# Kernel optimization log

Measured on AMD Instinct MI355X. Metric: run time of the kernel, lower is better.

## Reference

```python
import jax, jax.numpy as jnp
import numpy as np
from jax import lax
from jax.scipy.special import logsumexp

EPS = 0.01 ** 2      # blur^p, geomloss SamplesLoss(p=2, blur=0.01)
N_ITERS = 20         # fixed Sinkhorn iterations (log-domain)


def setup_inputs() -> dict:
    key = jax.random.key(0)
    k1, k2 = jax.random.split(key)
    p_q = jax.random.normal(k1, (4, 4096, 3), dtype=jnp.float32)
    p_gt = jax.random.normal(k2, (4, 4096, 4), dtype=jnp.float32)
    return {"p_q": p_q, "p_gt": p_gt}


def _cost(x, y):
    # C_ij = 0.5 * ||x_i - y_j||^2   (geomloss p=2 convention), [B,N,M]
    x2 = jnp.sum(x * x, -1)
    y2 = jnp.sum(y * y, -1)
    xy = jnp.einsum('bnd,bmd->bnm', x, y)
    return 0.5 * (x2[:, :, None] + y2[:, None, :] - 2.0 * xy)


def _softmin(C, pot, logw, axis):
    # -eps * logsumexp over `axis` of (pot - C)/eps + logw ; pot/logw broadcast on `axis`'s dual
    if axis == 2:
        z = (pot[:, None, :] - C) / EPS + logw  # reduce over M -> [B,N]
    else:
        z = (pot[:, :, None] - C) / EPS + logw  # reduce over N -> [B,M]
    return -EPS * logsumexp(z, axis=axis)


def _ot_potentials(C, loga, logb):
    # asymmetric log-domain Sinkhorn; iterate on detached cost (envelope theorem,
    # matching geomloss' detach-then-extrapolate gradient), final differentiable step.
    Cd = lax.stop_gradient(C)
    B, N, M = C.shape

    def body(i, fg):
        f, g = fg
        f = _softmin(Cd, g, logb, axis=2)
        g = _softmin(Cd, f, loga, axis=1)
        return (f, g)

    f0 = jnp.zeros((B, N), C.dtype)
    g0 = jnp.zeros((B, M), C.dtype)
    f, g = lax.fori_loop(0, N_ITERS, body, (f0, g0))
    fd, gd = lax.stop_gradient(f), lax.stop_gradient(g)
    f = _softmin(C, gd, logb, axis=2)
    g = _softmin(C, fd, loga, axis=1)
    return f, g


def _sym_potential(C, logw):
    # symmetric Sinkhorn for OT(a,a): single potential, damped updates
    Cd = lax.stop_gradient(C)
    B, N, _ = C.shape

    def body(i, f):
        return 0.5 * (f + _softmin(Cd, f, logw, axis=2))

    f = lax.fori_loop(0, N_ITERS, body, jnp.zeros((B, N), C.dtype))
    return _softmin(C, lax.stop_gradient(f), logw, axis=2)


def reference(p_q, p_gt):
    x = p_q                 # [B,N,3]
    y = p_gt[:, :, :3]      # [B,M,3]
    B, N, _ = x.shape
    M = y.shape[1]
    loga = jnp.full((1, 1), -jnp.log(N), x.dtype)  # uniform weights (broadcast)
    logb = jnp.full((1, 1), -jnp.log(M), x.dtype)

    Cxy = _cost(x, y)
    Cxx = _cost(x, x)
    Cyy = _cost(y, y)

    f_ab, g_ab = _ot_potentials(Cxy, loga[:, :, None] * 0 - jnp.log(N), logb)
    # note: loga used in softmin over N-axis needs [.., :, None] broadcast; build explicitly:
    loga_b = jnp.full((B, N, 1), -jnp.log(N), x.dtype)
    logb_b = jnp.full((B, 1, M), -jnp.log(M), x.dtype)
    f_ab = _softmin(Cxy, lax.stop_gradient(g_ab), logb_b, axis=2)  # idempotent re-extrapolation
    g_ab = _softmin(Cxy, lax.stop_gradient(f_ab), loga_b, axis=1)
    f_aa = _sym_potential(Cxx, jnp.full((B, 1, N), -jnp.log(N), x.dtype))
    g_bb = _sym_potential(Cyy, logb_b)

    # debiased Sinkhorn divergence per batch: <a, f_ab - f_aa> + <b, g_ab - g_bb>
    L = jnp.mean(f_ab - f_aa, axis=1) + jnp.mean(g_ab - g_bb, axis=1)
    return L
```

## Files before the change

### kernel.cpp

```cpp
#include <hip/hip_runtime.h>
#include <math.h>

#define NPTS 4096
#define NBATCH 4
#define BLOCK 512
#define RPW 8

static constexpr float KSCALE     = 1.4426950408889634f / 1e-4f;
static constexpr float INVK2      = 1.0f / (KSCALE * KSCALE);
static constexpr float EPSLN2     = 1e-4f * 0.6931471805599453f;
static constexpr float NEGEPSLOGW = 8.31776616671934e-4f;
static constexpr float THR        = 20.0f;

__device__ __forceinline__ float fexp2(float x){
#if __has_builtin(__builtin_amdgcn_exp2f)
  return __builtin_amdgcn_exp2f(x);
#else
  return exp2f(x);
#endif
}
__device__ __forceinline__ float flog2(float x){
#if __has_builtin(__builtin_amdgcn_logf)
  return __builtin_amdgcn_logf(x);
#else
  return log2f(x);
#endif
}
__device__ __forceinline__ float frl(float x){
  return __int_as_float(__builtin_amdgcn_readfirstlane(__float_as_int(x)));
}

__global__ __launch_bounds__(BLOCK, 4) void softmin_kernel(
    const float* __restrict__ rowA, int rsA, const float4* __restrict__ pkInA,
    float4* __restrict__ pkOutA, const float* __restrict__ hOldA,
    float* __restrict__ outA, int modeA,
    const float* __restrict__ rowB, int rsB, const float4* __restrict__ pkInB,
    float4* __restrict__ pkOutB, const float* __restrict__ hOldB,
    float* __restrict__ outB, int modeB)
{
  __shared__ float4 qs[NPTS];

  int bid = blockIdx.x;
  const float* rowp; const float4* pkin; float4* pkout; const float* hold;
  float* outp; int rs, mode;
  if (bid < 256) { rowp=rowA; pkin=pkInA; pkout=pkOutA; hold=hOldA; outp=outA; rs=rsA; mode=modeA; }
  else           { rowp=rowB; pkin=pkInB; pkout=pkOutB; hold=hOldB; outp=outB; rs=rsB; mode=modeB; }
  int lb = bid & 255;
  int b  = lb >> 6;
  int rb = lb & 63;

  int tid = threadIdx.x;
  int lane = tid & 63;
  int wu = __builtin_amdgcn_readfirstlane(tid >> 6);
  int r0 = rb*64 + wu*RPW;
  int ridx0 = b*NPTS + r0;

  {
    const float4* src = pkin + b*NPTS;
    #pragma unroll
    for (int i = 0; i < NPTS/BLOCK; ++i)
      qs[i*BLOCK + tid] = src[i*BLOCK + tid];
  }

  float sx[RPW], sy[RPW], sz[RPW];
  #pragma unroll
  for (int i = 0; i < RPW; ++i) {
    const float* p = rowp + (size_t)(ridx0 + i) * rs;
    sx[i] = frl(p[0]*KSCALE); sy[i] = frl(p[1]*KSCALE); sz[i] = frl(p[2]*KSCALE);
  }

  __syncthreads();

  float cmax[4][RPW];
  #pragma unroll
  for (int c = 0; c < 4; ++c)
    #pragma unroll
    for (int r = 0; r < RPW; ++r) cmax[c][r] = -INFINITY;

  #pragma unroll
  for (int c = 0; c < 4; ++c) {
    #pragma unroll
    for (int g = 0; g < 4; ++g) {
      int base = c*1024 + g*256 + lane;
      float4 q0 = qs[base], q1 = qs[base+64], q2 = qs[base+128], q3 = qs[base+192];
      #pragma unroll
      for (int r = 0; r < RPW; ++r) {
        float t0 = fmaf(sx[r],q0.x,fmaf(sy[r],q0.y,fmaf(sz[r],q0.z,q0.w)));
        float t1 = fmaf(sx[r],q1.x,fmaf(sy[r],q1.y,fmaf(sz[r],q1.z,q1.w)));
        float t2 = fmaf(sx[r],q2.x,fmaf(sy[r],q2.y,fmaf(sz[r],q2.z,q2.w)));
        float t3 = fmaf(sx[r],q3.x,fmaf(sy[r],q3.y,fmaf(sz[r],q3.z,q3.w)));
        float u  = fmaxf(fmaxf(t0,t1),t2);
        cmax[c][r] = fmaxf(fmaxf(u,t3),cmax[c][r]);
      }
    }
  }

  float M[RPW];
  #pragma unroll
  for (int r = 0; r < RPW; ++r) {
    float mm = fmaxf(fmaxf(cmax[0][r],cmax[1][r]), fmaxf(cmax[2][r],cmax[3][r]));
    #pragma unroll
    for (int off = 32; off; off >>= 1) mm = fmaxf(mm, __shfl_xor(mm, off, 64));
    M[r] = mm;
  }

  float S[RPW];
  #pragma unroll
  for (int r = 0; r < RPW; ++r) S[r] = 0.f;

  #pragma unroll
  for (int c = 0; c < 4; ++c) {
    int am = 0;
    #pragma unroll
    for (int r = 0; r < RPW; ++r)
      am |= __any(cmax[c][r] > M[r] - THR) ? (1 << r) : 0;
    if (am) {
      #pragma unroll
      for (int g = 0; g < 4; ++g) {
        int base = c*1024 + g*256 + lane;
        float4 q0 = qs[base], q1 = qs[base+64], q2 = qs[base+128], q3 = qs[base+192];
        #pragma unroll
        for (int r = 0; r < RPW; ++r) if (am & (1 << r)) {
          float t0 = fmaf(sx[r],q0.x,fmaf(sy[r],q0.y,fmaf(sz[r],q0.z,q0.w)));
          float t1 = fmaf(sx[r],q1.x,fmaf(sy[r],q1.y,fmaf(sz[r],q1.z,q1.w)));
          float t2 = fmaf(sx[r],q2.x,fmaf(sy[r],q2.y,fmaf(sz[r],q2.z,q2.w)));
          float t3 = fmaf(sx[r],q3.x,fmaf(sy[r],q3.y,fmaf(sz[r],q3.z,q3.w)));
          float u  = fmaxf(fmaxf(t0,t1),t2);
          float v  = fmaxf(u,t3);
          if (__any(v > M[r] - THR)) {
            float e0 = fexp2(t0-M[r]) + fexp2(t1-M[r]);
            float e1 = fexp2(t2-M[r]) + fexp2(t3-M[r]);
            S[r] += e0 + e1;
          }
        }
      }
    }
  }

  #pragma unroll
  for (int r = 0; r < RPW; ++r) {
    float s = S[r];
    #pragma unroll
    for (int off = 32; off; off >>= 1) s += __shfl_xor(s, off, 64);
    float ch = 0.5f*(sx[r]*sx[r] + sy[r]*sy[r] + sz[r]*sz[r]) * INVK2;
    float res = fmaf(-EPSLN2, M[r] + flog2(s), ch + NEGEPSLOGW);
    if (lane == r) {
      if (mode) res = 0.5f*(hold[ridx0 + r] + res);
      outp[ridx0 + r] = res;
      ((float*)(pkout + (ridx0 + r)))[3] = (res - ch) * KSCALE;
    }
  }
}

__global__ void pack_init(const float* __restrict__ x, const float* __restrict__ y,
                          float4* pkfab, float4* pkgab,
                          float4* pkfaa0, float4* pkfaa1,
                          float4* pkgbb0, float4* pkgbb1)
{
  int i = blockIdx.x*256 + threadIdx.x;
  const float* xp = x + (size_t)i*3;
  float xx = xp[0], xy = xp[1], xz = xp[2];
  float4 vx; vx.x=xx; vx.y=xy; vx.z=xz;
  vx.w = -0.5f*(xx*xx + xy*xy + xz*xz)*KSCALE;
  const float* yp = y + (size_t)i*4;
  float yx = yp[0], yy = yp[1], yz = yp[2];
  float4 vy; vy.x=yx; vy.y=yy; vy.z=yz;
  vy.w = -0.5f*(yx*yx + yy*yy + yz*yz)*KSCALE;
  pkgab[i]  = vx; pkfaa0[i] = vx; pkfaa1[i] = vx;
  pkfab[i]  = vy; pkgbb0[i] = vy; pkgbb1[i] = vy;
}

__global__ void reduce_kernel(const float* __restrict__ fab, const float* __restrict__ faa,
                              const float* __restrict__ gab, const float* __restrict__ gbb,
                              float* __restrict__ out)
{
  int b = blockIdx.x;
  int tid = threadIdx.x;
  float s = 0.f;
  for (int i = tid; i < NPTS; i += 256) {
    int idx = b*NPTS + i;
    s += (fab[idx] - faa[idx]) + (gab[idx] - gbb[idx]);
  }
  for (int off = 32; off > 0; off >>= 1) s += __shfl_down(s, off, 64);
  __shared__ float red[4];
  if ((tid & 63) == 0) red[tid >> 6] = s;
  __syncthreads();
  if (tid == 0) out[b] = (red[0]+red[1]+red[2]+red[3]) * (1.0f/NPTS);
}

extern "C" void kernel_launch(void* const* d_in, const int* in_sizes, int n_in,
                              void* d_out, int out_size, void* d_ws, size_t ws_size,
                              hipStream_t stream)
{
  const float* x = (const float*)d_in[0];
  const float* y = (const float*)d_in[1];
  float* ws = (float*)d_ws;
  const size_t P = (size_t)NBATCH * NPTS;

  float* f_ab    = ws + 0*P;
  float* g_ab    = ws + 1*P;
  float* faaR[2] = { ws + 2*P, ws + 4*P };
  float* gbbR[2] = { ws + 3*P, ws + 5*P };
  float4* pk4    = (float4*)(ws + 6*P);
  float4* PKfab    = pk4 + 0*P;
  float4* PKgab    = pk4 + 1*P;
  float4* PKfaa[2] = { pk4 + 2*P, pk4 + 3*P };
  float4* PKgbb[2] = { pk4 + 4*P, pk4 + 5*P };

  hipMemsetAsync(ws + 2*P, 0, 2*P*sizeof(float), stream);
  pack_init<<<dim3(P/256), dim3(256), 0, stream>>>(x, y, PKfab, PKgab,
                                                   PKfaa[0], PKfaa[1], PKgbb[0], PKgbb[1]);

  for (int i = 0; i < 21; ++i) {
    int cur = i & 1, nxt = cur ^ 1;
    int modeS = (i < 20) ? 1 : 0;
    softmin_kernel<<<512, BLOCK, 0, stream>>>(
        x, 3, PKfab, PKgab, f_ab, f_ab, 0,
        x, 3, PKfaa[cur], PKfaa[nxt], faaR[cur], faaR[nxt], modeS);
    softmin_kernel<<<512, BLOCK, 0, stream>>>(
        y, 4, PKgab, PKfab, g_ab, g_ab, 0,
        y, 4, PKgbb[cur], PKgbb[nxt], gbbR[cur], gbbR[nxt], modeS);
  }
  reduce_kernel<<<dim3(4), dim3(256), 0, stream>>>(f_ab, faaR[1], g_ab, gbbR[1], (float*)d_out);
}
```

Before: 1.013 ms.

## Use single-pass online softmin seeded by previous potential for symmetric blocks

Blocks handling the symmetric self-transport potentials (bid >= 256) now run a single pass. The running max is seeded from the previous potential plus the point's norm term, and an online rescaled logsumexp skips tiles whose values fall below the threshold. This replaces the separate max pass followed by an exp pass, cutting the dot-product work roughly in half for those blocks. The risk is that a loose initial max estimate adds rescale exps, and the lane-divergent online max needs a cross-lane rescale at the end.

After: 910.7 us, median of 2. 1.11x faster.

```diff
diff --git a/kernel.cpp b/kernel.cpp
--- a/kernel.cpp
+++ b/kernel.cpp
@@ -62,26 +62,108 @@
       qs[i*BLOCK + tid] = src[i*BLOCK + tid];
   }
 
-  float sx[RPW], sy[RPW], sz[RPW];
+  float sx[RPW], sy[RPW], sz[RPW], hh[RPW];
   #pragma unroll
   for (int i = 0; i < RPW; ++i) {
     const float* p = rowp + (size_t)(ridx0 + i) * rs;
     sx[i] = frl(p[0]*KSCALE); sy[i] = frl(p[1]*KSCALE); sz[i] = frl(p[2]*KSCALE);
+    hh[i] = frl(hold[ridx0 + i]);
   }
 
   __syncthreads();
 
-  float cmax[4][RPW];
-  #pragma unroll
-  for (int c = 0; c < 4; ++c)
-    #pragma unroll
-    for (int r = 0; r < RPW; ++r) cmax[c][r] = -INFINITY;
-
-  #pragma unroll
-  for (int c = 0; c < 4; ++c) {
-    #pragma unroll
-    for (int g = 0; g < 4; ++g) {
-      int base = c*1024 + g*256 + lane;
+  if (bid < 256) {
+    float cmax[4][RPW];
+    #pragma unroll
+    for (int c = 0; c < 4; ++c)
+      #pragma unroll
+      for (int r = 0; r < RPW; ++r) cmax[c][r] = -INFINITY;
+
+    #pragma unroll
+    for (int c = 0; c < 4; ++c) {
+      #pragma unroll
+      for (int g = 0; g < 4; ++g) {
+        int base = c*1024 + g*256 + lane;
+        float4 q0 = qs[base], q1 = qs[base+64], q2 = qs[base+128], q3 = qs[base+192];
+        #pragma unroll
+        for (int r = 0; r < RPW; ++r) {
+          float t0 = fmaf(sx[r],q0.x,fmaf(sy[r],q0.y,fmaf(sz[r],q0.z,q0.w)));
+          float t1 = fmaf(sx[r],q1.x,fmaf(sy[r],q1.y,fmaf(sz[r],q1.z,q1.w)));
+          float t2 = fmaf(sx[r],q2.x,fmaf(sy[r],q2.y,fmaf(sz[r],q2.z,q2.w)));
+          float t3 = fmaf(sx[r],q3.x,fmaf(sy[r],q3.y,fmaf(sz[r],q3.z,q3.w)));
+          float u  = fmaxf(fmaxf(t0,t1),t2);
+          cmax[c][r] = fmaxf(fmaxf(u,t3),cmax[c][r]);
+        }
+      }
+    }
+
+    float M[RPW];
+    #pragma unroll
+    for (int r = 0; r < RPW; ++r) {
+      float mm = fmaxf(fmaxf(cmax[0][r],cmax[1][r]), fmaxf(cmax[2][r],cmax[3][r]));
+      #pragma unroll
+      for (int off = 32; off; off >>= 1) mm = fmaxf(mm, __shfl_xor(mm, off, 64));
+      M[r] = mm;
+    }
+
+    float S[RPW];
+    #pragma unroll
+    for (int r = 0; r < RPW; ++r) S[r] = 0.f;
+
+    #pragma unroll
+    for (int c = 0; c < 4; ++c) {
+      int am = 0;
+      #pragma unroll
+      for (int r = 0; r < RPW; ++r)
+        am |= __any(cmax[c][r] > M[r] - THR) ? (1 << r) : 0;
+      if (am) {
+        #pragma unroll
+        for (int g = 0; g < 4; ++g) {
+          int base = c*1024 + g*256 + lane;
+          float4 q0 = qs[base], q1 = qs[base+64], q2 = qs[base+128], q3 = qs[base+192];
+          #pragma unroll
+          for (int r = 0; r < RPW; ++r) if (am & (1 << r)) {
+            float t0 = fmaf(sx[r],q0.x,fmaf(sy[r],q0.y,fmaf(sz[r],q0.z,q0.w)));
+            float t1 = fmaf(sx[r],q1.x,fmaf(sy[r],q1.y,fmaf(sz[r],q1.z,q1.w)));
+            float t2 = fmaf(sx[r],q2.x,fmaf(sy[r],q2.y,fmaf(sz[r],q2.z,q2.w)));
+            float t3 = fmaf(sx[r],q3.x,fmaf(sy[r],q3.y,fmaf(sz[r],q3.z,q3.w)));
+            float u  = fmaxf(fmaxf(t0,t1),t2);
+            float v  = fmaxf(u,t3);
+            if (__any(v > M[r] - THR)) {
+              float e0 = fexp2(t0-M[r]) + fexp2(t1-M[r]);
+              float e1 = fexp2(t2-M[r]) + fexp2(t3-M[r]);
+              S[r] += e0 + e1;
+            }
+          }
+        }
+      }
+    }
+
+    #pragma unroll
+    for (int r = 0; r < RPW; ++r) {
+      float s = S[r];
+      #pragma unroll
+      for (int off = 32; off; off >>= 1) s += __shfl_xor(s, off, 64);
+      float ch = 0.5f*(sx[r]*sx[r] + sy[r]*sy[r] + sz[r]*sz[r]) * INVK2;
+      float res = fmaf(-EPSLN2, M[r] + flog2(s), ch + NEGEPSLOGW);
+      if (lane == r) {
+        if (mode) res = 0.5f*(hh[r] + res);
+        outp[ridx0 + r] = res;
+        ((float*)(pkout + (ridx0 + r)))[3] = (res - ch) * KSCALE;
+      }
+    }
+  } else {
+    float M[RPW], S[RPW], chv[RPW];
+    #pragma unroll
+    for (int r = 0; r < RPW; ++r) {
+      chv[r] = 0.5f*(sx[r]*sx[r] + sy[r]*sy[r] + sz[r]*sz[r]) * INVK2;
+      M[r] = (hh[r] + chv[r]) * KSCALE;
+      S[r] = 0.f;
+    }
+
+    #pragma unroll
+    for (int g = 0; g < 16; ++g) {
+      int base = g*256 + lane;
       float4 q0 = qs[base], q1 = qs[base+64], q2 = qs[base+128], q3 = qs[base+192];
       #pragma unroll
       for (int r = 0; r < RPW; ++r) {
@@ -89,65 +171,33 @@
         float t1 = fmaf(sx[r],q1.x,fmaf(sy[r],q1.y,fmaf(sz[r],q1.z,q1.w)));
         float t2 = fmaf(sx[r],q2.x,fmaf(sy[r],q2.y,fmaf(sz[r],q2.z,q2.w)));
         float t3 = fmaf(sx[r],q3.x,fmaf(sy[r],q3.y,fmaf(sz[r],q3.z,q3.w)));
-        float u  = fmaxf(fmaxf(t0,t1),t2);
-        cmax[c][r] = fmaxf(fmaxf(u,t3),cmax[c][r]);
-      }
-    }
-  }
-
-  float M[RPW];
-  #pragma unroll
-  for (int r = 0; r < RPW; ++r) {
-    float mm = fmaxf(fmaxf(cmax[0][r],cmax[1][r]), fmaxf(cmax[2][r],cmax[3][r]));
-    #pragma unroll
-    for (int off = 32; off; off >>= 1) mm = fmaxf(mm, __shfl_xor(mm, off, 64));
-    M[r] = mm;
-  }
-
-  float S[RPW];
-  #pragma unroll
-  for (int r = 0; r < RPW; ++r) S[r] = 0.f;
-
-  #pragma unroll
-  for (int c = 0; c < 4; ++c) {
-    int am = 0;
-    #pragma unroll
-    for (int r = 0; r < RPW; ++r)
-      am |= __any(cmax[c][r] > M[r] - THR) ? (1 << r) : 0;
-    if (am) {
-      #pragma unroll
-      for (int g = 0; g < 4; ++g) {
-        int base = c*1024 + g*256 + lane;
-        float4 q0 = qs[base], q1 = qs[base+64], q2 = qs[base+128], q3 = qs[base+192];
-        #pragma unroll
-        for (int r = 0; r < RPW; ++r) if (am & (1 << r)) {
-          float t0 = fmaf(sx[r],q0.x,fmaf(sy[r],q0.y,fmaf(sz[r],q0.z,q0.w)));
-          float t1 = fmaf(sx[r],q1.x,fmaf(sy[r],q1.y,fmaf(sz[r],q1.z,q1.w)));
-          float t2 = fmaf(sx[r],q2.x,fmaf(sy[r],q2.y,fmaf(sz[r],q2.z,q2.w)));
-          float t3 = fmaf(sx[r],q3.x,fmaf(sy[r],q3.y,fmaf(sz[r],q3.z,q3.w)));
-          float u  = fmaxf(fmaxf(t0,t1),t2);
-          float v  = fmaxf(u,t3);
-          if (__any(v > M[r] - THR)) {
-            float e0 = fexp2(t0-M[r]) + fexp2(t1-M[r]);
-            float e1 = fexp2(t2-M[r]) + fexp2(t3-M[r]);
-            S[r] += e0 + e1;
-          }
+        float u    = fmaxf(fmaxf(t0,t1),t2);
+        float cmax = fmaxf(u,t3);
+        if (__any(cmax > M[r] - THR)) {
+          float Mn = fmaxf(M[r], cmax);
+          float sc = fexp2(M[r] - Mn);
+          float e0 = fexp2(t0-Mn) + fexp2(t1-Mn);
+          float e1 = fexp2(t2-Mn) + fexp2(t3-Mn);
+          S[r] = fmaf(S[r], sc, e0 + e1);
+          M[r] = Mn;
         }
       }
     }
-  }
-
-  #pragma unroll
-  for (int r = 0; r < RPW; ++r) {
-    float s = S[r];
-    #pragma unroll
-    for (int off = 32; off; off >>= 1) s += __shfl_xor(s, off, 64);
-    float ch = 0.5f*(sx[r]*sx[r] + sy[r]*sy[r] + sz[r]*sz[r]) * INVK2;
-    float res = fmaf(-EPSLN2, M[r] + flog2(s), ch + NEGEPSLOGW);
-    if (lane == r) {
-      if (mode) res = 0.5f*(hold[ridx0 + r] + res);
-      outp[ridx0 + r] = res;
-      ((float*)(pkout + (ridx0 + r)))[3] = (res - ch) * KSCALE;
+
+    #pragma unroll
+    for (int r = 0; r < RPW; ++r) {
+      float mm = M[r];
+      #pragma unroll
+      for (int off = 32; off; off >>= 1) mm = fmaxf(mm, __shfl_xor(mm, off, 64));
+      float s = S[r] * fexp2(M[r] - mm);
+      #pragma unroll
+      for (int off = 32; off; off >>= 1) s += __shfl_xor(s, off, 64);
+      float res = fmaf(-EPSLN2, mm + flog2(s), chv[r] + NEGEPSLOGW);
+      if (lane == r) {
+        if (mode) res = 0.5f*(hh[r] + res);
+        outp[ridx0 + r] = res;
+        ((float*)(pkout + (ridx0 + r)))[3] = (res - chv[r]) * KSCALE;
+      }
     }
   }
 }
```
